# Kernel tuning notes

Measured on AMD Instinct MI355X. Metric: run time of the kernel, lower is better.

The kernel has to match this reference:

```python
import jax, jax.numpy as jnp
import numpy as np

EPS = 1e-6


def setup_inputs() -> dict:
    key = jax.random.key(0)
    k1, k2, k3, k4 = jax.random.split(key, 4)
    B, L, H, E = 16, 4096, 8, 64
    return {
        "queries": jax.random.normal(k1, (B, L, H, E), dtype=jnp.float32),
        "keys": jax.random.normal(k2, (B, L, H, E), dtype=jnp.float32),
        "values": jax.random.normal(k3, (B, L, H, E), dtype=jnp.float32),
        "attn_mask": jnp.ones((1,), dtype=bool),
        "gamma": jax.random.uniform(k4, (1,), dtype=jnp.float32),
    }


def reference(queries, keys, values, attn_mask, gamma):
    # Faithful to the original: keys/values/attn_mask are unused; Q=K=V=queries.
    B, L, H, E = queries.shape
    HE = H * E
    V = queries.reshape(B, L, HE)              # raw values [B, L, HE]
    # l2_norm: normalize over dim=-2 (the L axis)
    Qn = V / jnp.linalg.norm(V, axis=-2, keepdims=True)   # [B, L, HE]
    Kt = jnp.swapaxes(Qn, -1, -2)              # K = l2_norm(K).permute -> [B, HE, L]
    # tailor_sum: 1 / (HE + sum_n Kt[b,n,l] * (sum_l' Qn[b,l',n] + eps))  -> [B, L]
    q_colsum = jnp.sum(Qn, axis=-2) + EPS      # [B, HE]
    tailor = 1.0 / (HE + jnp.einsum('bnl,bn->bl', Kt, q_colsum))  # [B, L]
    # value_sum over L, broadcast to [B, L, HE]
    value_sum = jnp.sum(V, axis=-2)            # [B, HE]
    # (V @ K) @ Q == V @ (K @ Q): use the linear-complexity [HE,HE] inner matrix
    KQ = jnp.einsum('bnl,blm->bnm', Kt, Qn)    # [B, HE, HE]
    part = jnp.einsum('bln,bnm->blm', V, KQ)   # [B, L, HE]
    matrix_sum = value_sum[:, None, :] + part  # [B, L, HE]
    weight_value = (matrix_sum * tailor[:, :, None]).reshape(B, L, H, E)
    return queries + gamma * weight_value
```

## Files before the change

kernel.cpp:

```cpp
#include <hip/hip_runtime.h>

#define EPS 1e-6f
#define LL 4096
#define HE 512

typedef __attribute__((ext_vector_type(8))) short short8;
typedef __attribute__((ext_vector_type(4))) float f32x4;

__device__ __forceinline__ unsigned short f2bf(float f) {
    union { float f; unsigned u; } v; v.f = f;
    unsigned r = v.u + 0x7FFFu + ((v.u >> 16) & 1u);
    return (unsigned short)(r >> 16);
}
__device__ __forceinline__ float bf2f(unsigned short s) {
    union { unsigned u; float f; } v; v.u = ((unsigned)s) << 16;
    return v.f;
}
__device__ __forceinline__ void gl16(const unsigned short* g, unsigned short* l) {
    __builtin_amdgcn_global_load_lds(
        (const __attribute__((address_space(1))) unsigned int*)(const void*)g,
        (__attribute__((address_space(3))) unsigned int*)(void*)l,
        16, 0, 0);
}

__global__ __launch_bounds__(256) void k1_stream(const float* __restrict__ q,
        unsigned short* __restrict__ Vb, float* __restrict__ ps,
        float* __restrict__ pq) {
    __shared__ float lds_s[4][512];
    __shared__ float lds_q[4][512];
    int blk = blockIdx.x;
    int b = blk >> 6, lt = blk & 63;
    int t = threadIdx.x;
    int oct = t & 63, w = t >> 6;
    size_t rowbase = (size_t)b * LL + lt * 64 + w * 16;
    const float* qb = q + rowbase * HE + oct * 8;
    unsigned short* vb = Vb + rowbase * HE + oct * 8;
    float s[8] = {}, qq[8] = {};
    #pragma unroll
    for (int r = 0; r < 16; r++) {
        float4 v0 = *(const float4*)(qb + (size_t)r * HE);
        float4 v1 = *(const float4*)(qb + (size_t)r * HE + 4);
        unsigned short e[8] = {f2bf(v0.x), f2bf(v0.y), f2bf(v0.z), f2bf(v0.w),
                               f2bf(v1.x), f2bf(v1.y), f2bf(v1.z), f2bf(v1.w)};
        short8 w8;
        #pragma unroll
        for (int c = 0; c < 8; c++) {
            w8[c] = (short)e[c];
            float x = bf2f(e[c]);
            s[c] += x; qq[c] += x * x;
        }
        *(short8*)(vb + (size_t)r * HE) = w8;
    }
    #pragma unroll
    for (int c = 0; c < 8; c++) {
        lds_s[w][oct * 8 + c] = s[c];
        lds_q[w][oct * 8 + c] = qq[c];
    }
    __syncthreads();
    #pragma unroll
    for (int h = 0; h < 2; h++) {
        int col = h * 256 + t;
        float ss = lds_s[0][col] + lds_s[1][col] + lds_s[2][col] + lds_s[3][col];
        float sq = lds_q[0][col] + lds_q[1][col] + lds_q[2][col] + lds_q[3][col];
        ps[(size_t)lt * 8192 + b * 512 + col] = ss;
        pq[(size_t)lt * 8192 + b * 512 + col] = sq;
    }
}

__global__ __launch_bounds__(256) void k2_reduce(const float* __restrict__ ps,
        const float* __restrict__ pq, float* __restrict__ sumV,
        float* __restrict__ cvec, float* __restrict__ invn) {
    int i = blockIdx.x * 256 + threadIdx.x;
    float s = 0.f, qq = 0.f;
    #pragma unroll 8
    for (int lt = 0; lt < 64; lt++) {
        s  += ps[(size_t)lt * 8192 + i];
        qq += pq[(size_t)lt * 8192 + i];
    }
    float inv = 1.0f / sqrtf(qq);
    sumV[i] = s;
    invn[i] = inv;
    cvec[i] = (s * inv + EPS) * inv;
}

__global__ __launch_bounds__(256) void k3_dvec(const unsigned short* __restrict__ Vb,
        const float* __restrict__ cvec, float* __restrict__ dvec) {
    int blk = blockIdx.x;
    int b = blk >> 7, lblk = blk & 127;
    int t = threadIdx.x;
    int lloc = t >> 3, j = t & 7;
    int l = lblk * 32 + lloc;
    const unsigned short* rowp = Vb + ((size_t)b * LL + l) * HE + j * 64;
    const float* cp = cvec + b * HE + j * 64;
    float d = 0.f;
    #pragma unroll
    for (int g = 0; g < 8; g++) {
        short8 v = *(const short8*)(rowp + g * 8);
        float4 c0 = *(const float4*)(cp + g * 8);
        float4 c1 = *(const float4*)(cp + g * 8 + 4);
        d += bf2f((unsigned short)v[0]) * c0.x + bf2f((unsigned short)v[1]) * c0.y
           + bf2f((unsigned short)v[2]) * c0.z + bf2f((unsigned short)v[3]) * c0.w
           + bf2f((unsigned short)v[4]) * c1.x + bf2f((unsigned short)v[5]) * c1.y
           + bf2f((unsigned short)v[6]) * c1.z + bf2f((unsigned short)v[7]) * c1.w;
    }
    d += __shfl_xor(d, 1); d += __shfl_xor(d, 2); d += __shfl_xor(d, 4);
    if (j == 0) dvec[(size_t)b * LL + l] = d;
}

__global__ __launch_bounds__(256) void k4_gram(const unsigned short* __restrict__ Vb,
        unsigned short* __restrict__ Gp) {
    __shared__ __attribute__((aligned(16))) unsigned short lt_a[128][72];
    __shared__ __attribute__((aligned(16))) unsigned short lt_b[128][72];
    int cpx = gridDim.x >> 3;
    int blk = ((int)blockIdx.x & 7) * cpx + ((int)blockIdx.x >> 3);
    int b = blk / 80;
    int rem = blk - b * 80;
    int pair = rem >> 3, split = rem & 7;
    int nt = (pair < 4) ? 0 : (pair < 7) ? 1 : (pair < 9) ? 2 : 3;
    int off = (nt * (9 - nt)) >> 1;
    int mt = nt + pair - off;
    bool diag = (nt == mt);
    int N0 = nt * 128, M0 = mt * 128;
    int t = threadIdx.x;
    int w = t >> 6, lane = t & 63;
    int wr = w >> 1, wc = w & 1;
    int lr = lane & 15, q4 = lane >> 4;
    int oct = t & 15;
    int l0 = (t >> 4) * 4;
    int lp = l0 ^ (8 * (oct & 7));
    const unsigned short* pa = Vb + ((size_t)b * LL + split * 512) * HE + N0 + oct * 8;
    const unsigned short* pb = Vb + ((size_t)b * LL + split * 512) * HE + M0 + oct * 8;
    f32x4 acc[4][4] = {};
    short8 ra[4], rb[4];

#define K4LOAD(KB) do { \
    _Pragma("unroll") \
    for (int r = 0; r < 4; r++) { \
        size_t ro = (size_t)((KB) * 64 + l0 + r) * HE; \
        ra[r] = *(const short8*)(pa + ro); \
        if (!diag) rb[r] = *(const short8*)(pb + ro); \
    } } while (0)

#define K4WRITE() do { \
    _Pragma("unroll") \
    for (int c = 0; c < 8; c++) { \
        uint2 da; \
        da.x = (unsigned)(unsigned short)ra[0][c] | ((unsigned)(unsigned short)ra[1][c] << 16); \
        da.y = (unsigned)(unsigned short)ra[2][c] | ((unsigned)(unsigned short)ra[3][c] << 16); \
        *(uint2*)&lt_a[oct * 8 + c][lp] = da; \
        if (!diag) { \
            uint2 db; \
            db.x = (unsigned)(unsigned short)rb[0][c] | ((unsigned)(unsigned short)rb[1][c] << 16); \
            db.y = (unsigned)(unsigned short)rb[2][c] | ((unsigned)(unsigned short)rb[3][c] << 16); \
            *(uint2*)&lt_b[oct * 8 + c][lp] = db; \
        } \
    } } while (0)

    K4LOAD(0);
    #pragma unroll
    for (int kb = 0; kb < 8; kb++) {
        if (kb) __builtin_amdgcn_s_barrier();
        K4WRITE();
        if (kb < 7) K4LOAD(kb + 1);
        asm volatile("s_waitcnt lgkmcnt(0)" ::: "memory");
        __builtin_amdgcn_s_barrier();
        #pragma unroll
        for (int ks = 0; ks < 2; ks++) {
            short8 af[4], bfr[4];
            #pragma unroll
            for (int i = 0; i < 4; i++) {
                int row = wr * 64 + i * 16 + lr;
                int col = (ks * 32 + q4 * 8) ^ (8 * ((2 * i + (lr >> 3)) & 7));
                af[i] = *(const short8*)&lt_a[row][col];
            }
            #pragma unroll
            for (int j = 0; j < 4; j++) {
                int row = wc * 64 + j * 16 + lr;
                int col = (ks * 32 + q4 * 8) ^ (8 * ((2 * j + (lr >> 3)) & 7));
                bfr[j] = diag ? *(const short8*)&lt_a[row][col]
                              : *(const short8*)&lt_b[row][col];
            }
            #pragma unroll
            for (int i = 0; i < 4; i++)
                #pragma unroll
                for (int j = 0; j < 4; j++)
                    acc[i][j] = __builtin_amdgcn_mfma_f32_16x16x32_bf16(af[i], bfr[j], acc[i][j], 0, 0, 0);
        }
    }
#undef K4LOAD
#undef K4WRITE
    size_t tbase = ((size_t)(b * 10 + pair) * 8 + split) * 16384;
    #pragma unroll
    for (int i = 0; i < 4; i++) {
        int nb = wr * 64 + i * 16 + q4 * 4;
        #pragma unroll
        for (int j = 0; j < 4; j++) {
            int ml = wc * 64 + j * 16 + lr;
            ushort4 wv;
            wv.x = f2bf(acc[i][j][0]); wv.y = f2bf(acc[i][j][1]);
            wv.z = f2bf(acc[i][j][2]); wv.w = f2bf(acc[i][j][3]);
            *(ushort4*)&Gp[tbase + (size_t)ml * 128 + nb] = wv;
        }
    }
}

__global__ __launch_bounds__(256) void k5_reduce(const unsigned short* __restrict__ Gp,
        const float* __restrict__ invn, unsigned short* __restrict__ KQb) {
    __shared__ unsigned short lds_t[128][130];
    int blk = blockIdx.x;
    int b = blk / 10, pair = blk % 10;
    int nt = (pair < 4) ? 0 : (pair < 7) ? 1 : (pair < 9) ? 2 : 3;
    int off = (nt * (9 - nt)) >> 1;
    int mt = nt + pair - off;
    int N0 = nt * 128, M0 = mt * 128;
    int t = threadIdx.x;
    const unsigned short* gp = Gp + ((size_t)(b * 10 + pair) * 8) * 16384;
    const float* inb = invn + (size_t)b * HE;
    #pragma unroll 2
    for (int e = 0; e < 32; e++) {
        int idx = e * 512 + t * 2;
        int ml = idx >> 7, nl = idx & 127;
        float s0 = 0.f, s1 = 0.f;
        #pragma unroll
        for (int sp = 0; sp < 8; sp++) {
            unsigned g2 = *(const unsigned*)&gp[(size_t)sp * 16384 + idx];
            s0 += bf2f((unsigned short)(g2 & 0xFFFF));
            s1 += bf2f((unsigned short)(g2 >> 16));
        }
        float im = inb[M0 + ml];
        ushort2 v;
        v.x = f2bf(s0 * inb[N0 + nl] * im);
        v.y = f2bf(s1 * inb[N0 + nl + 1] * im);
        *(ushort2*)&KQb[((size_t)b * HE + M0 + ml) * HE + N0 + nl] = v;
        *(ushort2*)&lds_t[ml][nl] = v;
    }
    __syncthreads();
    #pragma unroll 2
    for (int e = 0; e < 32; e++) {
        int idx = e * 512 + t * 2;
        int nl = idx >> 7, ml = idx & 127;
        ushort2 v;
        v.x = lds_t[ml][nl];
        v.y = lds_t[ml + 1][nl];
        *(ushort2*)&KQb[((size_t)b * HE + N0 + nl) * HE + M0 + ml] = v;
    }
}

__global__ __launch_bounds__(256) void k6_part(const unsigned short* __restrict__ KQb,
        const unsigned short* __restrict__ Vb, const float* __restrict__ dvec,
        const float* __restrict__ sumV, const float* __restrict__ gamma,
        float* __restrict__ out) {
    __shared__ __attribute__((aligned(16))) unsigned short la[2][128][64];
    __shared__ __attribute__((aligned(16))) unsigned short lb[2][128][64];
    int cpx = gridDim.x >> 3;
    int blk = ((int)blockIdx.x & 7) * cpx + ((int)blockIdx.x >> 3);
    int b = blk >> 7, mt = (blk >> 5) & 3, lt = blk & 31;
    int M0 = mt * 128, L0 = lt * 128;
    int t = threadIdx.x;
    int w = t >> 6, lane = t & 63;
    int wr = w >> 1, wc = w & 1;
    int rl = lane >> 3;
    int cl = ((lane & 7) ^ rl) << 3;
    int lr = lane & 15, q4 = lane >> 4;
    int ch0 = (q4 ^ (lane & 7)) << 3;
    const unsigned short* pa = KQb + ((size_t)b * HE + M0) * HE;
    const unsigned short* pb = Vb + ((size_t)b * LL + L0) * HE;
    float gma = gamma[0];
    f32x4 acc[4][4] = {};

#define STAGE6(B, KB) do { \
    int _k0 = (KB) * 64; \
    _Pragma("unroll") \
    for (int p = 0; p < 4; p++) { \
        int r0 = p * 32 + w * 8; \
        gl16(pa + (size_t)(r0 + rl) * HE + _k0 + cl, &la[B][r0][0]); \
        gl16(pb + (size_t)(r0 + rl) * HE + _k0 + cl, &lb[B][r0][0]); \
    } } while (0)

    STAGE6(0, 0);
    #pragma unroll
    for (int kb = 0; kb < 8; kb++) {
        int cur = kb & 1;
        if (kb < 7) {
            STAGE6(cur ^ 1, kb + 1);
            asm volatile("s_waitcnt vmcnt(8)" ::: "memory");
        } else {
            asm volatile("s_waitcnt vmcnt(0)" ::: "memory");
        }
        __builtin_amdgcn_s_barrier();
        #pragma unroll
        for (int ks = 0; ks < 2; ks++) {
            int colA = ch0 ^ (ks << 5);
            short8 af[4], bfr[4];
            #pragma unroll
            for (int i = 0; i < 4; i++)
                af[i] = *(const short8*)&la[cur][wr*64 + i*16 + lr][colA];
            #pragma unroll
            for (int j = 0; j < 4; j++)
                bfr[j] = *(const short8*)&lb[cur][wc*64 + j*16 + lr][colA];
            #pragma unroll
            for (int i = 0; i < 4; i++)
                #pragma unroll
                for (int j = 0; j < 4; j++)
                    acc[i][j] = __builtin_amdgcn_mfma_f32_16x16x32_bf16(af[i], bfr[j], acc[i][j], 0, 0, 0);
        }
        __builtin_amdgcn_s_barrier();
    }
#undef STAGE6
    #pragma unroll
    for (int j = 0; j < 4; j++) {
        int lglob = L0 + wc*64 + j*16 + lr;
        float dt = dvec[(size_t)b * LL + lglob];
        float tailor = 1.0f / (512.0f + dt);
        #pragma unroll
        for (int i = 0; i < 4; i++) {
            int m4 = M0 + wr*64 + i*16 + q4*4;
            size_t ofs = ((size_t)b * LL + lglob) * HE + m4;
            ushort4 rv = *(const ushort4*)(Vb + ((size_t)b * LL + lglob) * HE + m4);
            float4 vs = *(const float4*)(sumV + (size_t)b * HE + m4);
            float4 o;
            o.x = bf2f(rv.x) + gma * (vs.x + acc[i][j][0]) * tailor;
            o.y = bf2f(rv.y) + gma * (vs.y + acc[i][j][1]) * tailor;
            o.z = bf2f(rv.z) + gma * (vs.z + acc[i][j][2]) * tailor;
            o.w = bf2f(rv.w) + gma * (vs.w + acc[i][j][3]) * tailor;
            *(float4*)(out + ofs) = o;
        }
    }
}

extern "C" void kernel_launch(void* const* d_in, const int* in_sizes, int n_in,
                              void* d_out, int out_size, void* d_ws, size_t ws_size,
                              hipStream_t stream) {
    const float* q     = (const float*)d_in[0];
    const float* gamma = (const float*)d_in[4];
    float* out = (float*)d_out;
    char* ws = (char*)d_ws;
    float* sumV  = (float*)(ws);
    float* cvec  = (float*)(ws + 65536);
    float* invn  = (float*)(ws + 98304);
    float* dvec  = (float*)(ws + 131072);
    unsigned short* KQb = (unsigned short*)(ws + 524288);
    unsigned short* Vb  = (unsigned short*)(ws + 8912896);
    unsigned short* Gp  = (unsigned short*)(ws + 76021760);
    float* ps = (float*)(ws + 117964800);
    float* pq = (float*)(ws + 120061952);

    k1_stream<<<1024, 256, 0, stream>>>(q, Vb, ps, pq);
    k2_reduce<<<32,   256, 0, stream>>>(ps, pq, sumV, cvec, invn);
    k3_dvec  <<<2048, 256, 0, stream>>>(Vb, cvec, dvec);
    k4_gram  <<<1280, 256, 0, stream>>>(Vb, Gp);
    k5_reduce<<<160,  256, 0, stream>>>(Gp, invn, KQb);
    k6_part  <<<2048, 256, 0, stream>>>(KQb, Vb, dvec, sumV, gamma, out);
}
```

Before: 203.7 us.

## Double-buffer LDS tiles and register prefetch in Gram kernel

The Gram (V^T V) kernel now keeps two LDS buffers and two register staging sets. Each iteration writes the next tile to the alternate LDS buffer and issues global loads two tiles ahead while MFMAs consume the current buffer, with one barrier per iteration instead of two. This aims to hide global-load and LDS-write latency behind compute. In exchange it doubles LDS use (about 73KB per block) and register staging, which may lower occupancy.

```diff
diff --git a/kernel.cpp b/kernel.cpp
--- a/kernel.cpp
+++ b/kernel.cpp
@@ -109,8 +109,8 @@
 
 __global__ __launch_bounds__(256) void k4_gram(const unsigned short* __restrict__ Vb,
         unsigned short* __restrict__ Gp) {
-    __shared__ __attribute__((aligned(16))) unsigned short lt_a[128][72];
-    __shared__ __attribute__((aligned(16))) unsigned short lt_b[128][72];
+    __shared__ __attribute__((aligned(16))) unsigned short lt_a[2][128][72];
+    __shared__ __attribute__((aligned(16))) unsigned short lt_b[2][128][72];
     int cpx = gridDim.x >> 3;
     int blk = ((int)blockIdx.x & 7) * cpx + ((int)blockIdx.x >> 3);
     int b = blk / 80;
@@ -131,39 +131,42 @@
     const unsigned short* pa = Vb + ((size_t)b * LL + split * 512) * HE + N0 + oct * 8;
     const unsigned short* pb = Vb + ((size_t)b * LL + split * 512) * HE + M0 + oct * 8;
     f32x4 acc[4][4] = {};
-    short8 ra[4], rb[4];
-
-#define K4LOAD(KB) do { \
+    short8 ra[2][4], rb[2][4];
+
+#define K4LOAD(KB, SET) do { \
     _Pragma("unroll") \
     for (int r = 0; r < 4; r++) { \
         size_t ro = (size_t)((KB) * 64 + l0 + r) * HE; \
-        ra[r] = *(const short8*)(pa + ro); \
-        if (!diag) rb[r] = *(const short8*)(pb + ro); \
+        ra[SET][r] = *(const short8*)(pa + ro); \
+        if (!diag) rb[SET][r] = *(const short8*)(pb + ro); \
     } } while (0)
 
-#define K4WRITE() do { \
+#define K4WRITE(SET, BUF) do { \
     _Pragma("unroll") \
     for (int c = 0; c < 8; c++) { \
         uint2 da; \
-        da.x = (unsigned)(unsigned short)ra[0][c] | ((unsigned)(unsigned short)ra[1][c] << 16); \
-        da.y = (unsigned)(unsigned short)ra[2][c] | ((unsigned)(unsigned short)ra[3][c] << 16); \
-        *(uint2*)&lt_a[oct * 8 + c][lp] = da; \
+        da.x = (unsigned)(unsigned short)ra[SET][0][c] | ((unsigned)(unsigned short)ra[SET][1][c] << 16); \
+        da.y = (unsigned)(unsigned short)ra[SET][2][c] | ((unsigned)(unsigned short)ra[SET][3][c] << 16); \
+        *(uint2*)&lt_a[BUF][oct * 8 + c][lp] = da; \
         if (!diag) { \
             uint2 db; \
-            db.x = (unsigned)(unsigned short)rb[0][c] | ((unsigned)(unsigned short)rb[1][c] << 16); \
-            db.y = (unsigned)(unsigned short)rb[2][c] | ((unsigned)(unsigned short)rb[3][c] << 16); \
-            *(uint2*)&lt_b[oct * 8 + c][lp] = db; \
+            db.x = (unsigned)(unsigned short)rb[SET][0][c] | ((unsigned)(unsigned short)rb[SET][1][c] << 16); \
+            db.y = (unsigned)(unsigned short)rb[SET][2][c] | ((unsigned)(unsigned short)rb[SET][3][c] << 16); \
+            *(uint2*)&lt_b[BUF][oct * 8 + c][lp] = db; \
         } \
     } } while (0)
 
-    K4LOAD(0);
+    K4LOAD(0, 0);
+    K4WRITE(0, 0);
+    K4LOAD(1, 1);
     #pragma unroll
     for (int kb = 0; kb < 8; kb++) {
-        if (kb) __builtin_amdgcn_s_barrier();
-        K4WRITE();
-        if (kb < 7) K4LOAD(kb + 1);
+        const int cur = kb & 1;
         asm volatile("s_waitcnt lgkmcnt(0)" ::: "memory");
         __builtin_amdgcn_s_barrier();
+        asm volatile("" ::: "memory");
+        if (kb < 7) K4WRITE(cur ^ 1, cur ^ 1);
+        if (kb < 6) K4LOAD(kb + 2, cur);
         #pragma unroll
         for (int ks = 0; ks < 2; ks++) {
             short8 af[4], bfr[4];
@@ -171,14 +174,14 @@
             for (int i = 0; i < 4; i++) {
                 int row = wr * 64 + i * 16 + lr;
                 int col = (ks * 32 + q4 * 8) ^ (8 * ((2 * i + (lr >> 3)) & 7));
-                af[i] = *(const short8*)&lt_a[row][col];
+                af[i] = *(const short8*)&lt_a[cur][row][col];
             }
             #pragma unroll
             for (int j = 0; j < 4; j++) {
                 int row = wc * 64 + j * 16 + lr;
                 int col = (ks * 32 + q4 * 8) ^ (8 * ((2 * j + (lr >> 3)) & 7));
-                bfr[j] = diag ? *(const short8*)&lt_a[row][col]
-                              : *(const short8*)&lt_b[row][col];
+                bfr[j] = diag ? *(const short8*)&lt_a[cur][row][col]
+                              : *(const short8*)&lt_b[cur][row][col];
             }
             #pragma unroll
             for (int i = 0; i < 4; i++)
```

Result: no change. 203.6 us (-0.1%).

## Write transposed bf16 copy in stream kernel and async-load it in gram kernel

Applied to the files above, without the earlier changes.

The first kernel now also writes a transposed bf16 copy of V ([B, HE, L]), transposing through swizzled shared memory. The Gram kernel reads this transposed layout directly into double-buffered LDS with global_load_lds, which removes the register-level transpose and the LDS write loop and lets the next tile load overlap the MFMA work. The cost is an extra 64 MB of global writes in the first kernel and a larger workspace.

```diff
diff --git a/kernel.cpp b/kernel.cpp
--- a/kernel.cpp
+++ b/kernel.cpp
@@ -23,9 +23,10 @@
         16, 0, 0);
 }
 
-__global__ __launch_bounds__(256) void k1_stream(const float* __restrict__ q,
-        unsigned short* __restrict__ Vb, float* __restrict__ ps,
-        float* __restrict__ pq) {
+__global__ __launch_bounds__(256) void k1_fuse2(const float* __restrict__ q,
+        unsigned short* __restrict__ Vb, unsigned short* __restrict__ Vt,
+        float* __restrict__ ps, float* __restrict__ pq) {
+    __shared__ unsigned short ldsT[256][68];
     __shared__ float lds_s[4][512];
     __shared__ float lds_q[4][512];
     int blk = blockIdx.x;
@@ -35,6 +36,7 @@
     size_t rowbase = (size_t)b * LL + lt * 64 + w * 16;
     const float* qb = q + rowbase * HE + oct * 8;
     unsigned short* vb = Vb + rowbase * HE + oct * 8;
+    short8 rows[16];
     float s[8] = {}, qq[8] = {};
     #pragma unroll
     for (int r = 0; r < 16; r++) {
@@ -49,6 +51,7 @@
             float x = bf2f(e[c]);
             s[c] += x; qq[c] += x * x;
         }
+        rows[r] = w8;
         *(short8*)(vb + (size_t)r * HE) = w8;
     }
     #pragma unroll
@@ -64,6 +67,41 @@
         float sq = lds_q[0][col] + lds_q[1][col] + lds_q[2][col] + lds_q[3][col];
         ps[(size_t)lt * 8192 + b * 512 + col] = ss;
         pq[(size_t)lt * 8192 + b * 512 + col] = sq;
+    }
+    int gg = (t & 63) >> 3, oo = t & 7;
+    #pragma unroll
+    for (int h = 0; h < 2; h++) {
+        __syncthreads();
+        if ((oct >> 5) == h) {
+            int ol = oct & 31;
+            #pragma unroll
+            for (int c = 0; c < 8; c++) {
+                int n1 = ol * 8 + c;
+                int swz = (ol & 7) * 8;
+                #pragma unroll
+                for (int g = 0; g < 4; g++) {
+                    uint2 dv;
+                    dv.x = (unsigned)(unsigned short)rows[g*4+0][c]
+                         | ((unsigned)(unsigned short)rows[g*4+1][c] << 16);
+                    dv.y = (unsigned)(unsigned short)rows[g*4+2][c]
+                         | ((unsigned)(unsigned short)rows[g*4+3][c] << 16);
+                    int lp = (w * 16 + g * 4) ^ swz;
+                    *(uint2*)&ldsT[n1][lp] = dv;
+                }
+            }
+        }
+        __syncthreads();
+        #pragma unroll
+        for (int it = 0; it < 8; it++) {
+            int n1 = w * 64 + it * 8 + gg;
+            int swz = ((n1 >> 3) & 7) * 8;
+            int l0 = oo * 8;
+            uint2 a0 = *(const uint2*)&ldsT[n1][(l0    ) ^ swz];
+            uint2 a1 = *(const uint2*)&ldsT[n1][(l0 + 4) ^ swz];
+            uint4 uv; uv.x = a0.x; uv.y = a0.y; uv.z = a1.x; uv.w = a1.y;
+            unsigned short* dst = Vt + ((size_t)b * HE + h * 256 + n1) * LL + lt * 64 + l0;
+            *(uint4*)dst = uv;
+        }
     }
 }
 
@@ -107,10 +145,10 @@
     if (j == 0) dvec[(size_t)b * LL + l] = d;
 }
 
-__global__ __launch_bounds__(256) void k4_gram(const unsigned short* __restrict__ Vb,
+__global__ __launch_bounds__(256) void k4_gram(const unsigned short* __restrict__ Vt,
         unsigned short* __restrict__ Gp) {
-    __shared__ __attribute__((aligned(16))) unsigned short lt_a[128][72];
-    __shared__ __attribute__((aligned(16))) unsigned short lt_b[128][72];
+    __shared__ __attribute__((aligned(16))) unsigned short la[2][128][64];
+    __shared__ __attribute__((aligned(16))) unsigned short lb[2][128][64];
     int cpx = gridDim.x >> 3;
     int blk = ((int)blockIdx.x & 7) * cpx + ((int)blockIdx.x >> 3);
     int b = blk / 80;
@@ -124,78 +162,63 @@
     int t = threadIdx.x;
     int w = t >> 6, lane = t & 63;
     int wr = w >> 1, wc = w & 1;
+    int rl = lane >> 3;
+    int cl = ((lane & 7) ^ rl) << 3;
     int lr = lane & 15, q4 = lane >> 4;
-    int oct = t & 15;
-    int l0 = (t >> 4) * 4;
-    int lp = l0 ^ (8 * (oct & 7));
-    const unsigned short* pa = Vb + ((size_t)b * LL + split * 512) * HE + N0 + oct * 8;
-    const unsigned short* pb = Vb + ((size_t)b * LL + split * 512) * HE + M0 + oct * 8;
+    int ch0 = (q4 ^ (lane & 7)) << 3;
+    const unsigned short* pa = Vt + ((size_t)b * HE + N0) * LL + split * 512;
+    const unsigned short* pb = Vt + ((size_t)b * HE + M0) * LL + split * 512;
     f32x4 acc[4][4] = {};
-    short8 ra[4], rb[4];
-
-#define K4LOAD(KB) do { \
+
+#define STAGE4(B, KB) do { \
+    int _k0 = (KB) * 64; \
     _Pragma("unroll") \
-    for (int r = 0; r < 4; r++) { \
-        size_t ro = (size_t)((KB) * 64 + l0 + r) * HE; \
-        ra[r] = *(const short8*)(pa + ro); \
-        if (!diag) rb[r] = *(const short8*)(pb + ro); \
+    for (int p = 0; p < 4; p++) { \
+        int r0 = p * 32 + w * 8; \
+        gl16(pa + (size_t)(r0 + rl) * LL + _k0 + cl, &la[B][r0][0]); \
+        if (!diag) gl16(pb + (size_t)(r0 + rl) * LL + _k0 + cl, &lb[B][r0][0]); \
     } } while (0)
 
-#define K4WRITE() do { \
-    _Pragma("unroll") \
-    for (int c = 0; c < 8; c++) { \
-        uint2 da; \
-        da.x = (unsigned)(unsigned short)ra[0][c] | ((unsigned)(unsigned short)ra[1][c] << 16); \
-        da.y = (unsigned)(unsigned short)ra[2][c] | ((unsigned)(unsigned short)ra[3][c] << 16); \
-        *(uint2*)&lt_a[oct * 8 + c][lp] = da; \
-        if (!diag) { \
-            uint2 db; \
-            db.x = (unsigned)(unsigned short)rb[0][c] | ((unsigned)(unsigned short)rb[1][c] << 16); \
-            db.y = (unsigned)(unsigned short)rb[2][c] | ((unsigned)(unsigned short)rb[3][c] << 16); \
-            *(uint2*)&lt_b[oct * 8 + c][lp] = db; \
-        } \
-    } } while (0)
-
-    K4LOAD(0);
+    STAGE4(0, 0);
     #pragma unroll
     for (int kb = 0; kb < 8; kb++) {
-        if (kb) __builtin_amdgcn_s_barrier();
-        K4WRITE();
-        if (kb < 7) K4LOAD(kb + 1);
-        asm volatile("s_waitcnt lgkmcnt(0)" ::: "memory");
+        int cur = kb & 1;
+        if (kb < 7) {
+            STAGE4(cur ^ 1, kb + 1);
+            if (diag) { asm volatile("s_waitcnt vmcnt(4)" ::: "memory"); }
+            else      { asm volatile("s_waitcnt vmcnt(8)" ::: "memory"); }
+        } else {
+            asm volatile("s_waitcnt vmcnt(0)" ::: "memory");
+        }
         __builtin_amdgcn_s_barrier();
+        const unsigned short (*A)[64] = la[cur];
+        const unsigned short (*Bp)[64] = diag ? la[cur] : lb[cur];
         #pragma unroll
         for (int ks = 0; ks < 2; ks++) {
+            int colA = ch0 ^ (ks << 5);
             short8 af[4], bfr[4];
             #pragma unroll
-            for (int i = 0; i < 4; i++) {
-                int row = wr * 64 + i * 16 + lr;
-                int col = (ks * 32 + q4 * 8) ^ (8 * ((2 * i + (lr >> 3)) & 7));
-                af[i] = *(const short8*)&lt_a[row][col];
-            }
-            #pragma unroll
-            for (int j = 0; j < 4; j++) {
-                int row = wc * 64 + j * 16 + lr;
-                int col = (ks * 32 + q4 * 8) ^ (8 * ((2 * j + (lr >> 3)) & 7));
-                bfr[j] = diag ? *(const short8*)&lt_a[row][col]
-                              : *(const short8*)&lt_b[row][col];
-            }
+            for (int i = 0; i < 4; i++)
+                af[i] = *(const short8*)&A[wr*64 + i*16 + lr][colA];
+            #pragma unroll
+            for (int j = 0; j < 4; j++)
+                bfr[j] = *(const short8*)&Bp[wc*64 + j*16 + lr][colA];
             #pragma unroll
             for (int i = 0; i < 4; i++)
                 #pragma unroll
                 for (int j = 0; j < 4; j++)
                     acc[i][j] = __builtin_amdgcn_mfma_f32_16x16x32_bf16(af[i], bfr[j], acc[i][j], 0, 0, 0);
         }
-    }
-#undef K4LOAD
-#undef K4WRITE
+        __builtin_amdgcn_s_barrier();
+    }
+#undef STAGE4
     size_t tbase = ((size_t)(b * 10 + pair) * 8 + split) * 16384;
     #pragma unroll
     for (int i = 0; i < 4; i++) {
-        int nb = wr * 64 + i * 16 + q4 * 4;
+        int nb = wr*64 + i*16 + q4*4;
         #pragma unroll
         for (int j = 0; j < 4; j++) {
-            int ml = wc * 64 + j * 16 + lr;
+            int ml = wc*64 + j*16 + lr;
             ushort4 wv;
             wv.x = f2bf(acc[i][j][0]); wv.y = f2bf(acc[i][j][1]);
             wv.z = f2bf(acc[i][j][2]); wv.w = f2bf(acc[i][j][3]);
@@ -340,15 +363,16 @@
     float* invn  = (float*)(ws + 98304);
     float* dvec  = (float*)(ws + 131072);
     unsigned short* KQb = (unsigned short*)(ws + 524288);
-    unsigned short* Vb  = (unsigned short*)(ws + 8912896);
-    unsigned short* Gp  = (unsigned short*)(ws + 76021760);
-    float* ps = (float*)(ws + 117964800);
-    float* pq = (float*)(ws + 120061952);
-
-    k1_stream<<<1024, 256, 0, stream>>>(q, Vb, ps, pq);
+    unsigned short* Vt  = (unsigned short*)(ws + 8912896);
+    unsigned short* Vb  = (unsigned short*)(ws + 76021760);
+    unsigned short* Gp  = (unsigned short*)(ws + 143130624);
+    float* ps = (float*)(ws + 185073664);
+    float* pq = (float*)(ws + 187170816);
+
+    k1_fuse2 <<<1024, 256, 0, stream>>>(q, Vb, Vt, ps, pq);
     k2_reduce<<<32,   256, 0, stream>>>(ps, pq, sumV, cvec, invn);
     k3_dvec  <<<2048, 256, 0, stream>>>(Vb, cvec, dvec);
-    k4_gram  <<<1280, 256, 0, stream>>>(Vb, Gp);
+    k4_gram  <<<1280, 256, 0, stream>>>(Vt, Gp);
     k5_reduce<<<160,  256, 0, stream>>>(Gp, invn, KQb);
     k6_part  <<<2048, 256, 0, stream>>>(KQb, Vb, dvec, sumV, gamma, out);
 }
```

Result: slower. 209.5 us (+2.8%).

## Fuse tailor dot-product into output GEMM and use transposed LDS reads in Gram

Applied to the files above, without the earlier changes.

Removes the separate k3_dvec pass. The per-row dot product with cvec is now computed inside k6_part from the V tiles already staged in LDS, which saves a full re-read of Vb and one kernel launch. k4_gram is also restructured to stage tiles with direct global-to-LDS loads, double-buffered, and to build MFMA fragments with ds_read_b64_tr_b16 transposed reads. This replaces the old register repack and scattered LDS writes. The costs are extra LDS work and ALU inside k6, and the correctness of the new transpose addressing in k4 is a risk.

```diff
diff --git a/kernel.cpp b/kernel.cpp
--- a/kernel.cpp
+++ b/kernel.cpp
@@ -6,6 +6,8 @@
 
 typedef __attribute__((ext_vector_type(8))) short short8;
 typedef __attribute__((ext_vector_type(4))) float f32x4;
+typedef __attribute__((ext_vector_type(2))) unsigned u32x2;
+typedef __attribute__((ext_vector_type(4))) unsigned u32x4;
 
 __device__ __forceinline__ unsigned short f2bf(float f) {
     union { float f; unsigned u; } v; v.f = f;
@@ -22,6 +24,13 @@
         (__attribute__((address_space(3))) unsigned int*)(void*)l,
         16, 0, 0);
 }
+__device__ __forceinline__ unsigned lds_addr(const void* p) {
+    return (unsigned)(unsigned long long)(const __attribute__((address_space(3))) char*)p;
+}
+#define TRREAD(dst, addr, IMM) \
+    asm volatile("ds_read_b64_tr_b16 %0, %1 offset:%2" : "=v"(dst) : "v"(addr), "i"(IMM))
+
+union S8U { u32x4 u; short8 s; };
 
 __global__ __launch_bounds__(256) void k1_stream(const float* __restrict__ q,
         unsigned short* __restrict__ Vb, float* __restrict__ ps,
@@ -83,34 +92,10 @@
     cvec[i] = (s * inv + EPS) * inv;
 }
 
-__global__ __launch_bounds__(256) void k3_dvec(const unsigned short* __restrict__ Vb,
-        const float* __restrict__ cvec, float* __restrict__ dvec) {
-    int blk = blockIdx.x;
-    int b = blk >> 7, lblk = blk & 127;
-    int t = threadIdx.x;
-    int lloc = t >> 3, j = t & 7;
-    int l = lblk * 32 + lloc;
-    const unsigned short* rowp = Vb + ((size_t)b * LL + l) * HE + j * 64;
-    const float* cp = cvec + b * HE + j * 64;
-    float d = 0.f;
-    #pragma unroll
-    for (int g = 0; g < 8; g++) {
-        short8 v = *(const short8*)(rowp + g * 8);
-        float4 c0 = *(const float4*)(cp + g * 8);
-        float4 c1 = *(const float4*)(cp + g * 8 + 4);
-        d += bf2f((unsigned short)v[0]) * c0.x + bf2f((unsigned short)v[1]) * c0.y
-           + bf2f((unsigned short)v[2]) * c0.z + bf2f((unsigned short)v[3]) * c0.w
-           + bf2f((unsigned short)v[4]) * c1.x + bf2f((unsigned short)v[5]) * c1.y
-           + bf2f((unsigned short)v[6]) * c1.z + bf2f((unsigned short)v[7]) * c1.w;
-    }
-    d += __shfl_xor(d, 1); d += __shfl_xor(d, 2); d += __shfl_xor(d, 4);
-    if (j == 0) dvec[(size_t)b * LL + l] = d;
-}
-
 __global__ __launch_bounds__(256) void k4_gram(const unsigned short* __restrict__ Vb,
         unsigned short* __restrict__ Gp) {
-    __shared__ __attribute__((aligned(16))) unsigned short lt_a[128][72];
-    __shared__ __attribute__((aligned(16))) unsigned short lt_b[128][72];
+    __shared__ __attribute__((aligned(16))) unsigned short la[2][8192];
+    __shared__ __attribute__((aligned(16))) unsigned short lb[2][8192];
     int cpx = gridDim.x >> 3;
     int blk = ((int)blockIdx.x & 7) * cpx + ((int)blockIdx.x >> 3);
     int b = blk / 80;
@@ -125,70 +110,71 @@
     int w = t >> 6, lane = t & 63;
     int wr = w >> 1, wc = w & 1;
     int lr = lane & 15, q4 = lane >> 4;
-    int oct = t & 15;
-    int l0 = (t >> 4) * 4;
-    int lp = l0 ^ (8 * (oct & 7));
-    const unsigned short* pa = Vb + ((size_t)b * LL + split * 512) * HE + N0 + oct * 8;
-    const unsigned short* pb = Vb + ((size_t)b * LL + split * 512) * HE + M0 + oct * 8;
+    int srcRow = (lane >> 1) & 3;
+    int srcCol = (lane >> 3) * 16 + (lane & 1) * 8;
+    const unsigned short* pa = Vb + ((size_t)b * LL + split * 512) * HE + N0;
+    const unsigned short* pb = Vb + ((size_t)b * LL + split * 512) * HE + M0;
+    unsigned laneTr = (unsigned)((lane >> 4) * 2048 + (lane & 15) * 8);
+    unsigned rdA0 = lds_addr(&la[0][0]) + wr * 512 + laneTr;
+    unsigned rdA1 = lds_addr(&la[1][0]) + wr * 512 + laneTr;
+    unsigned rdB0 = (diag ? lds_addr(&la[0][0]) : lds_addr(&lb[0][0])) + wc * 512 + laneTr;
+    unsigned rdB1 = (diag ? lds_addr(&la[1][0]) : lds_addr(&lb[1][0])) + wc * 512 + laneTr;
     f32x4 acc[4][4] = {};
-    short8 ra[4], rb[4];
-
-#define K4LOAD(KB) do { \
+
+#define STG(B, KB) do { \
     _Pragma("unroll") \
-    for (int r = 0; r < 4; r++) { \
-        size_t ro = (size_t)((KB) * 64 + l0 + r) * HE; \
-        ra[r] = *(const short8*)(pa + ro); \
-        if (!diag) rb[r] = *(const short8*)(pb + ro); \
+    for (int lg = 0; lg < 4; lg++) { \
+        size_t ro = (size_t)((KB) * 64 + w * 16 + lg * 4 + srcRow) * HE + srcCol; \
+        gl16(pa + ro, &la[B][(w * 4 + lg) * 512]); \
+        if (!diag) gl16(pb + ro, &lb[B][(w * 4 + lg) * 512]); \
     } } while (0)
 
-#define K4WRITE() do { \
+#define FRAGS_MFMA(KS, AADDR, BADDR) do { \
+    u32x2 a0[4], a1[4], b0[4], b1[4]; \
+    TRREAD(a0[0], AADDR, (KS)*8192 + 0*128);        TRREAD(a1[0], AADDR, (KS)*8192 + 0*128 + 1024); \
+    TRREAD(a0[1], AADDR, (KS)*8192 + 1*128);        TRREAD(a1[1], AADDR, (KS)*8192 + 1*128 + 1024); \
+    TRREAD(a0[2], AADDR, (KS)*8192 + 2*128);        TRREAD(a1[2], AADDR, (KS)*8192 + 2*128 + 1024); \
+    TRREAD(a0[3], AADDR, (KS)*8192 + 3*128);        TRREAD(a1[3], AADDR, (KS)*8192 + 3*128 + 1024); \
+    TRREAD(b0[0], BADDR, (KS)*8192 + 0*128);        TRREAD(b1[0], BADDR, (KS)*8192 + 0*128 + 1024); \
+    TRREAD(b0[1], BADDR, (KS)*8192 + 1*128);        TRREAD(b1[1], BADDR, (KS)*8192 + 1*128 + 1024); \
+    TRREAD(b0[2], BADDR, (KS)*8192 + 2*128);        TRREAD(b1[2], BADDR, (KS)*8192 + 2*128 + 1024); \
+    TRREAD(b0[3], BADDR, (KS)*8192 + 3*128);        TRREAD(b1[3], BADDR, (KS)*8192 + 3*128 + 1024); \
+    asm volatile("s_waitcnt lgkmcnt(0)" ::: "memory"); \
+    __builtin_amdgcn_sched_barrier(0); \
+    short8 af[4], bfr[4]; \
     _Pragma("unroll") \
-    for (int c = 0; c < 8; c++) { \
-        uint2 da; \
-        da.x = (unsigned)(unsigned short)ra[0][c] | ((unsigned)(unsigned short)ra[1][c] << 16); \
-        da.y = (unsigned)(unsigned short)ra[2][c] | ((unsigned)(unsigned short)ra[3][c] << 16); \
-        *(uint2*)&lt_a[oct * 8 + c][lp] = da; \
-        if (!diag) { \
-            uint2 db; \
-            db.x = (unsigned)(unsigned short)rb[0][c] | ((unsigned)(unsigned short)rb[1][c] << 16); \
-            db.y = (unsigned)(unsigned short)rb[2][c] | ((unsigned)(unsigned short)rb[3][c] << 16); \
-            *(uint2*)&lt_b[oct * 8 + c][lp] = db; \
-        } \
-    } } while (0)
-
-    K4LOAD(0);
+    for (int i = 0; i < 4; i++) { \
+        S8U ua; ua.u = (u32x4){a0[i].x, a0[i].y, a1[i].x, a1[i].y}; af[i] = ua.s; \
+        S8U ub; ub.u = (u32x4){b0[i].x, b0[i].y, b1[i].x, b1[i].y}; bfr[i] = ub.s; \
+    } \
+    _Pragma("unroll") \
+    for (int i = 0; i < 4; i++) \
+        _Pragma("unroll") \
+        for (int j = 0; j < 4; j++) \
+            acc[i][j] = __builtin_amdgcn_mfma_f32_16x16x32_bf16(af[i], bfr[j], acc[i][j], 0, 0, 0); \
+    } while (0)
+
+    STG(0, 0);
     #pragma unroll
     for (int kb = 0; kb < 8; kb++) {
-        if (kb) __builtin_amdgcn_s_barrier();
-        K4WRITE();
-        if (kb < 7) K4LOAD(kb + 1);
-        asm volatile("s_waitcnt lgkmcnt(0)" ::: "memory");
+        int cur = kb & 1;
+        if (kb < 7) {
+            STG(cur ^ 1, kb + 1);
+            if (diag) { asm volatile("s_waitcnt vmcnt(4)" ::: "memory"); }
+            else      { asm volatile("s_waitcnt vmcnt(8)" ::: "memory"); }
+        } else {
+            asm volatile("s_waitcnt vmcnt(0)" ::: "memory");
+        }
         __builtin_amdgcn_s_barrier();
-        #pragma unroll
-        for (int ks = 0; ks < 2; ks++) {
-            short8 af[4], bfr[4];
-            #pragma unroll
-            for (int i = 0; i < 4; i++) {
-                int row = wr * 64 + i * 16 + lr;
-                int col = (ks * 32 + q4 * 8) ^ (8 * ((2 * i + (lr >> 3)) & 7));
-                af[i] = *(const short8*)&lt_a[row][col];
-            }
-            #pragma unroll
-            for (int j = 0; j < 4; j++) {
-                int row = wc * 64 + j * 16 + lr;
-                int col = (ks * 32 + q4 * 8) ^ (8 * ((2 * j + (lr >> 3)) & 7));
-                bfr[j] = diag ? *(const short8*)&lt_a[row][col]
-                              : *(const short8*)&lt_b[row][col];
-            }
-            #pragma unroll
-            for (int i = 0; i < 4; i++)
-                #pragma unroll
-                for (int j = 0; j < 4; j++)
-                    acc[i][j] = __builtin_amdgcn_mfma_f32_16x16x32_bf16(af[i], bfr[j], acc[i][j], 0, 0, 0);
-        }
-    }
-#undef K4LOAD
-#undef K4WRITE
+        __builtin_amdgcn_sched_barrier(0);
+        unsigned aAd = cur ? rdA1 : rdA0;
+        unsigned bAd = cur ? rdB1 : rdB0;
+        FRAGS_MFMA(0, aAd, bAd);
+        FRAGS_MFMA(1, aAd, bAd);
+        __builtin_amdgcn_s_barrier();
+    }
+#undef STG
+#undef FRAGS_MFMA
     size_t tbase = ((size_t)(b * 10 + pair) * 8 + split) * 16384;
     #pragma unroll
     for (int i = 0; i < 4; i++) {
@@ -247,11 +233,13 @@
 }
 
 __global__ __launch_bounds__(256) void k6_part(const unsigned short* __restrict__ KQb,
-        const unsigned short* __restrict__ Vb, const float* __restrict__ dvec,
+        const unsigned short* __restrict__ Vb, const float* __restrict__ cvec,
         const float* __restrict__ sumV, const float* __restrict__ gamma,
         float* __restrict__ out) {
     __shared__ __attribute__((aligned(16))) unsigned short la[2][128][64];
     __shared__ __attribute__((aligned(16))) unsigned short lb[2][128][64];
+    __shared__ float lds_c[512];
+    __shared__ float lds_d[128][2];
     int cpx = gridDim.x >> 3;
     int blk = ((int)blockIdx.x & 7) * cpx + ((int)blockIdx.x >> 3);
     int b = blk >> 7, mt = (blk >> 5) & 3, lt = blk & 31;
@@ -266,7 +254,12 @@
     const unsigned short* pa = KQb + ((size_t)b * HE + M0) * HE;
     const unsigned short* pb = Vb + ((size_t)b * LL + L0) * HE;
     float gma = gamma[0];
+    lds_c[t]       = cvec[b * HE + t];
+    lds_c[t + 256] = cvec[b * HE + t + 256];
+    __syncthreads();
     f32x4 acc[4][4] = {};
+    float dpart = 0.f;
+    int drow = t >> 1, dsw = (t >> 1) & 7, dh = t & 1;
 
 #define STAGE6(B, KB) do { \
     int _k0 = (KB) * 64; \
@@ -288,6 +281,19 @@
             asm volatile("s_waitcnt vmcnt(0)" ::: "memory");
         }
         __builtin_amdgcn_s_barrier();
+        {
+            int k0 = kb * 64;
+            #pragma unroll
+            for (int ch = 0; ch < 4; ch++) {
+                int g = dh * 4 + ch;
+                short8 v = *(const short8*)&lb[cur][drow][(g ^ dsw) << 3];
+                const float* cp = &lds_c[k0 + g * 8];
+                dpart += bf2f((unsigned short)v[0]) * cp[0] + bf2f((unsigned short)v[1]) * cp[1]
+                       + bf2f((unsigned short)v[2]) * cp[2] + bf2f((unsigned short)v[3]) * cp[3]
+                       + bf2f((unsigned short)v[4]) * cp[4] + bf2f((unsigned short)v[5]) * cp[5]
+                       + bf2f((unsigned short)v[6]) * cp[6] + bf2f((unsigned short)v[7]) * cp[7];
+            }
+        }
         #pragma unroll
         for (int ks = 0; ks < 2; ks++) {
             int colA = ch0 ^ (ks << 5);
@@ -307,10 +313,13 @@
         __builtin_amdgcn_s_barrier();
     }
 #undef STAGE6
+    lds_d[drow][dh] = dpart;
+    __syncthreads();
     #pragma unroll
     for (int j = 0; j < 4; j++) {
-        int lglob = L0 + wc*64 + j*16 + lr;
-        float dt = dvec[(size_t)b * LL + lglob];
+        int lloc = wc*64 + j*16 + lr;
+        int lglob = L0 + lloc;
+        float dt = lds_d[lloc][0] + lds_d[lloc][1];
         float tailor = 1.0f / (512.0f + dt);
         #pragma unroll
         for (int i = 0; i < 4; i++) {
@@ -338,7 +347,6 @@
     float* sumV  = (float*)(ws);
     float* cvec  = (float*)(ws + 65536);
     float* invn  = (float*)(ws + 98304);
-    float* dvec  = (float*)(ws + 131072);
     unsigned short* KQb = (unsigned short*)(ws + 524288);
     unsigned short* Vb  = (unsigned short*)(ws + 8912896);
     unsigned short* Gp  = (unsigned short*)(ws + 76021760);
@@ -347,8 +355,7 @@
 
     k1_stream<<<1024, 256, 0, stream>>>(q, Vb, ps, pq);
     k2_reduce<<<32,   256, 0, stream>>>(ps, pq, sumV, cvec, invn);
-    k3_dvec  <<<2048, 256, 0, stream>>>(Vb, cvec, dvec);
     k4_gram  <<<1280, 256, 0, stream>>>(Vb, Gp);
     k5_reduce<<<160,  256, 0, stream>>>(Gp, invn, KQb);
-    k6_part  <<<2048, 256, 0, stream>>>(KQb, Vb, dvec, sumV, gamma, out);
-}
+    k6_part  <<<2048, 256, 0, stream>>>(KQb, Vb, cvec, sumV, gamma, out);
+}
```

Result: slower. 210.4 us (+3.3%).
